# Optimization experiments

Measured on AMD Instinct MI355X. Metric: run time of the kernel, lower is better.

## Reference

```python
import jax, jax.numpy as jnp
import numpy as np

N, K, D = 1000000, 4, 16

def setup_inputs() -> dict:
    key = jax.random.key(0)
    k1, k2, k3, k4, k5 = jax.random.split(key, 5)
    z = jax.random.normal(k1, (N, D), dtype=jnp.float32)
    phi = jax.nn.softmax(jax.random.normal(k2, (K,), dtype=jnp.float32))  # mixture weights, sum to 1
    mu = jax.random.normal(k3, (K, D), dtype=jnp.float32)
    # Upper-triangular Cholesky-like factor with positive diagonal (module calls
    # solve_triangular(..., upper=True), i.e. L is treated as upper triangular).
    A = jax.random.normal(k4, (K, D, D), dtype=jnp.float32) * 0.1
    diag = 0.8 + 0.4 * jax.random.uniform(k5, (K, D), dtype=jnp.float32)
    L = jnp.triu(A, 1) + jnp.zeros((K, D, D), jnp.float32).at[:, jnp.arange(D), jnp.arange(D)].set(diag)
    return {"z": z, "phi": phi, "mu": mu, "L": L}

def reference(z, phi, mu, L):
    # z: [N,D], phi: [K], mu: [K,D], L: [K,D,D] upper-triangular
    z_centered = z[:, None, :] - mu[None, :, :]            # [N,K,D]
    b = jnp.transpose(z_centered, (1, 2, 0))               # [K,D,N]
    v = jax.lax.linalg.triangular_solve(L, b, left_side=True, lower=False)  # [K,D,N]
    log_det_sigma = 2.0 * jnp.sum(jnp.log(jnp.diagonal(L, axis1=-2, axis2=-1)), axis=1)  # [K]
    d = z.shape[1]
    logits = jnp.log(phi)[:, None] - 0.5 * (
        jnp.sum(jnp.square(v), axis=1)                     # [K,N] Mahalanobis term
        + d * jnp.log(2.0 * jnp.pi)
        + log_det_sigma[:, None]
    )                                                      # [K,N]
    energies = -jax.scipy.special.logsumexp(logits, axis=0)  # [N]
    return energies
```

## Files before the change

kernel.cpp:

```cpp
#include <hip/hip_runtime.h>
#include <math.h>

namespace {

constexpr int KK = 4;
constexpr int DD = 16;
constexpr int BLOCK = 256;
constexpr int PTS = 4;
constexpr float LOG2PI = 1.8378770664093453f;

__global__ __launch_bounds__(BLOCK)
void gmm_energy(const float* __restrict__ z, const float* __restrict__ phi,
                const float* __restrict__ mu, const float* __restrict__ L,
                float* __restrict__ out, int N)
{
    __shared__ float sLinv[KK][DD][DD];
    __shared__ float sW[KK][DD];
    __shared__ float sC0[KK];

    const int tid = threadIdx.x;

    if (tid < KK * DD) {
        const int k = tid >> 4;
        const int j = tid & 15;
        const float* Lk = L + k * DD * DD;
        float xv[DD];
        #pragma unroll
        for (int m = 0; m < DD; ++m) xv[m] = 0.0f;
        #pragma unroll
        for (int i = DD - 1; i >= 0; --i) {
            float s = (i == j) ? 1.0f : 0.0f;
            #pragma unroll
            for (int m = i + 1; m < DD; ++m)
                s -= Lk[i * DD + m] * xv[m];
            xv[i] = (i <= j) ? (s / Lk[i * DD + i]) : 0.0f;
        }
        #pragma unroll
        for (int i = 0; i < DD; ++i)
            sLinv[k][i][j] = xv[i];
    }
    __syncthreads();
    if (tid < KK * DD) {
        const int k = tid >> 4;
        const int i = tid & 15;
        float w = 0.0f;
        #pragma unroll
        for (int j = 0; j < DD; ++j)
            w += sLinv[k][i][j] * mu[k * DD + j];
        sW[k][i] = w;
    }
    if (tid < KK) {
        float logdet = 0.0f;
        #pragma unroll
        for (int i = 0; i < DD; ++i)
            logdet += __logf(L[tid * DD * DD + i * DD + i]);
        sC0[tid] = __logf(phi[tid]) - 8.0f * LOG2PI - logdet;
    }
    __syncthreads();

    const int base = blockIdx.x * (BLOCK * PTS) + tid * PTS;

    float zr[PTS][DD];
    if (base + PTS <= N) {
        #pragma unroll
        for (int p = 0; p < PTS; ++p) {
            const float4* zp = reinterpret_cast<const float4*>(z + (size_t)(base + p) * DD);
            #pragma unroll
            for (int c = 0; c < 4; ++c) {
                float4 v = zp[c];
                zr[p][c * 4 + 0] = v.x;
                zr[p][c * 4 + 1] = v.y;
                zr[p][c * 4 + 2] = v.z;
                zr[p][c * 4 + 3] = v.w;
            }
        }
    } else {
        #pragma unroll
        for (int p = 0; p < PTS; ++p) {
            if (base + p < N) {
                const float4* zp = reinterpret_cast<const float4*>(z + (size_t)(base + p) * DD);
                #pragma unroll
                for (int c = 0; c < 4; ++c) {
                    float4 v = zp[c];
                    zr[p][c * 4 + 0] = v.x;
                    zr[p][c * 4 + 1] = v.y;
                    zr[p][c * 4 + 2] = v.z;
                    zr[p][c * 4 + 3] = v.w;
                }
            } else {
                #pragma unroll
                for (int d = 0; d < DD; ++d) zr[p][d] = 0.0f;
            }
        }
    }

    float lg[PTS][KK];
    #pragma unroll
    for (int k = 0; k < KK; ++k) {
        float q[PTS];
        #pragma unroll
        for (int p = 0; p < PTS; ++p) q[p] = 0.0f;
        #pragma unroll
        for (int i = 0; i < DD; ++i) {
            const float wk = sW[k][i];
            float acc[PTS];
            #pragma unroll
            for (int p = 0; p < PTS; ++p) acc[p] = -wk;
            #pragma unroll
            for (int j = i; j < DD; ++j) {
                const float cf = sLinv[k][i][j];
                #pragma unroll
                for (int p = 0; p < PTS; ++p)
                    acc[p] = fmaf(cf, zr[p][j], acc[p]);
            }
            #pragma unroll
            for (int p = 0; p < PTS; ++p)
                q[p] = fmaf(acc[p], acc[p], q[p]);
        }
        const float c0 = sC0[k];
        #pragma unroll
        for (int p = 0; p < PTS; ++p)
            lg[p][k] = fmaf(-0.5f, q[p], c0);
    }

    float e[PTS];
    #pragma unroll
    for (int p = 0; p < PTS; ++p) {
        float m01 = fmaxf(lg[p][0], lg[p][1]);
        float m23 = fmaxf(lg[p][2], lg[p][3]);
        float m = fmaxf(m01, m23);
        float s = __expf(lg[p][0] - m) + __expf(lg[p][1] - m)
                + __expf(lg[p][2] - m) + __expf(lg[p][3] - m);
        e[p] = -(m + __logf(s));
    }

    if (base + PTS <= N) {
        float4 res;
        res.x = e[0]; res.y = e[1]; res.z = e[2]; res.w = e[3];
        *reinterpret_cast<float4*>(out + base) = res;
    } else {
        #pragma unroll
        for (int p = 0; p < PTS; ++p) {
            if (base + p < N) out[base + p] = e[p];
        }
    }
}

}

extern "C" void kernel_launch(void* const* d_in, const int* in_sizes, int n_in,
                              void* d_out, int out_size, void* d_ws, size_t ws_size,
                              hipStream_t stream) {
    const float* z   = (const float*)d_in[0];
    const float* phi = (const float*)d_in[1];
    const float* mu  = (const float*)d_in[2];
    const float* L   = (const float*)d_in[3];
    float* out = (float*)d_out;
    const int N = in_sizes[0] / DD;
    const int grid = (N + BLOCK * PTS - 1) / (BLOCK * PTS);
    gmm_energy<<<grid, BLOCK, 0, stream>>>(z, phi, mu, L, out, N);
}
```

Baseline: 111.3 us.

## Issue z loads before per-block L inversion and merge setup barriers

The global loads of z are moved ahead of the per-block triangular inversion of L, so their memory latency overlaps the setup arithmetic. The two setup barriers are merged into one, and each thread now computes its mu-projection entry right after the inversion. Division is replaced by a reciprocal intrinsic, the -0.5 factor is folded into Linv through a 1/sqrt2 scale, and an occupancy hint is added to launch bounds. Reading sLinv rows written by other lanes with no barrier in between relies on wavefront lockstep ordering, which is a correctness risk.

New measurement: 115.8 us. 4.1% more time.

```diff
diff --git a/kernel.cpp b/kernel.cpp
--- a/kernel.cpp
+++ b/kernel.cpp
@@ -8,8 +8,9 @@
 constexpr int BLOCK = 256;
 constexpr int PTS = 4;
 constexpr float LOG2PI = 1.8378770664093453f;
+constexpr float INV_SQRT2 = 0.70710678118654752f;
 
-__global__ __launch_bounds__(BLOCK)
+__global__ __launch_bounds__(BLOCK, 4)
 void gmm_energy(const float* __restrict__ z, const float* __restrict__ phi,
                 const float* __restrict__ mu, const float* __restrict__ L,
                 float* __restrict__ out, int N)
@@ -19,45 +20,6 @@
     __shared__ float sC0[KK];
 
     const int tid = threadIdx.x;
-
-    if (tid < KK * DD) {
-        const int k = tid >> 4;
-        const int j = tid & 15;
-        const float* Lk = L + k * DD * DD;
-        float xv[DD];
-        #pragma unroll
-        for (int m = 0; m < DD; ++m) xv[m] = 0.0f;
-        #pragma unroll
-        for (int i = DD - 1; i >= 0; --i) {
-            float s = (i == j) ? 1.0f : 0.0f;
-            #pragma unroll
-            for (int m = i + 1; m < DD; ++m)
-                s -= Lk[i * DD + m] * xv[m];
-            xv[i] = (i <= j) ? (s / Lk[i * DD + i]) : 0.0f;
-        }
-        #pragma unroll
-        for (int i = 0; i < DD; ++i)
-            sLinv[k][i][j] = xv[i];
-    }
-    __syncthreads();
-    if (tid < KK * DD) {
-        const int k = tid >> 4;
-        const int i = tid & 15;
-        float w = 0.0f;
-        #pragma unroll
-        for (int j = 0; j < DD; ++j)
-            w += sLinv[k][i][j] * mu[k * DD + j];
-        sW[k][i] = w;
-    }
-    if (tid < KK) {
-        float logdet = 0.0f;
-        #pragma unroll
-        for (int i = 0; i < DD; ++i)
-            logdet += __logf(L[tid * DD * DD + i * DD + i]);
-        sC0[tid] = __logf(phi[tid]) - 8.0f * LOG2PI - logdet;
-    }
-    __syncthreads();
-
     const int base = blockIdx.x * (BLOCK * PTS) + tid * PTS;
 
     float zr[PTS][DD];
@@ -94,6 +56,47 @@
         }
     }
 
+    if (tid < KK * DD) {
+        const int k = tid >> 4;
+        const int j = tid & 15;
+        const float* __restrict__ Lk = L + k * DD * DD;
+
+        float rd[DD];
+        #pragma unroll
+        for (int i = 0; i < DD; ++i)
+            rd[i] = __builtin_amdgcn_rcpf(Lk[i * DD + i]);
+
+        float xv[DD];
+        #pragma unroll
+        for (int m = 0; m < DD; ++m) xv[m] = 0.0f;
+        #pragma unroll
+        for (int i = DD - 1; i >= 0; --i) {
+            float s = (i == j) ? 1.0f : 0.0f;
+            #pragma unroll
+            for (int m = i + 1; m < DD; ++m)
+                s = fmaf(-Lk[i * DD + m], xv[m], s);
+            xv[i] = (i <= j) ? (s * rd[i]) : 0.0f;
+        }
+        #pragma unroll
+        for (int i = 0; i < DD; ++i)
+            sLinv[k][i][j] = xv[i] * INV_SQRT2;
+
+        const int i2 = j;
+        float w = 0.0f;
+        #pragma unroll
+        for (int jj = 0; jj < DD; ++jj)
+            w = fmaf(sLinv[k][i2][jj], mu[k * DD + jj], w);
+        sW[k][i2] = w;
+    }
+    if (tid < KK) {
+        float logdet = 0.0f;
+        #pragma unroll
+        for (int i = 0; i < DD; ++i)
+            logdet += __logf(L[tid * DD * DD + i * DD + i]);
+        sC0[tid] = __logf(phi[tid]) - 8.0f * LOG2PI - logdet;
+    }
+    __syncthreads();
+
     float lg[PTS][KK];
     #pragma unroll
     for (int k = 0; k < KK; ++k) {
@@ -103,11 +106,13 @@
         #pragma unroll
         for (int i = 0; i < DD; ++i) {
             const float wk = sW[k][i];
+            const float cdiag = sLinv[k][i][i];
             float acc[PTS];
             #pragma unroll
-            for (int p = 0; p < PTS; ++p) acc[p] = -wk;
+            for (int p = 0; p < PTS; ++p)
+                acc[p] = fmaf(cdiag, zr[p][i], -wk);
             #pragma unroll
-            for (int j = i; j < DD; ++j) {
+            for (int j = i + 1; j < DD; ++j) {
                 const float cf = sLinv[k][i][j];
                 #pragma unroll
                 for (int p = 0; p < PTS; ++p)
@@ -120,7 +125,7 @@
         const float c0 = sC0[k];
         #pragma unroll
         for (int p = 0; p < PTS; ++p)
-            lg[p][k] = fmaf(-0.5f, q[p], c0);
+            lg[p][k] = c0 - q[p];
     }
 
     float e[PTS];
```
